# Kernel optimization log

Hardware: AMD Instinct MI355X
Metric: run time of the kernel (lower is better)

The kernel has to match this reference:

```python
import jax, jax.numpy as jnp
import numpy as np

NUM_CLASSES = 10
P_CUTOFF = 0.95
TEMP = 0.5  # temperature used throughout the original forward
B_LB, B_ULB, D = 4096, 6144, 128


def _l2_normalize(x, eps=1e-12):
    # matches torch.nn.functional.normalize(x, dim=1)
    n = jnp.linalg.norm(x, axis=1, keepdims=True)
    return x / jnp.maximum(n, eps)


def setup_inputs() -> dict:
    key = jax.random.key(0)
    k = jax.random.split(key, 6)
    anchor_feat = jax.random.normal(k[0], (B_ULB, D), jnp.float32)
    positive_feat = jax.random.normal(k[1], (B_ULB, D), jnp.float32)
    lb_feat = jax.random.normal(k[2], (B_LB, D), jnp.float32)
    labels = jax.random.randint(k[3], (B_LB,), 0, NUM_CLASSES)
    lb_one_hot = jax.nn.one_hot(labels, NUM_CLASSES, dtype=jnp.float32)
    # scale logits so a realistic fraction of unlabeled samples pass the 0.95 cutoff
    logits_x_ulb_1 = 3.0 * jax.random.normal(k[4], (B_ULB, NUM_CLASSES), jnp.float32)
    logits_x_ulb_2 = 3.0 * jax.random.normal(k[5], (B_ULB, NUM_CLASSES), jnp.float32)
    return {
        "anchor_feat": anchor_feat,
        "positive_feat": positive_feat,
        "lb_feat": lb_feat,
        "lb_one_hot": lb_one_hot,
        "logits_x_ulb_1": logits_x_ulb_1,
        "logits_x_ulb_2": logits_x_ulb_2,
    }


def reference(anchor_feat, positive_feat, lb_feat, lb_one_hot,
              logits_x_ulb_1, logits_x_ulb_2):
    # pick the more-confident view per unlabeled sample
    prob1 = jax.nn.softmax(logits_x_ulb_1 / TEMP, axis=1)
    prob2 = jax.nn.softmax(logits_x_ulb_2 / TEMP, axis=1)
    take1 = jnp.max(prob1, axis=-1) >= jnp.max(prob2, axis=-1)
    logits_gt = jnp.where(take1[:, None], logits_x_ulb_1, logits_x_ulb_2)

    # confidence mask at p_cutoff = 0.95
    mask = (jax.nn.softmax(logits_gt, axis=1) >= P_CUTOFF).astype(logits_gt.dtype)
    logits_gt = logits_gt * mask

    # per-class counts: labeled via one-hot sum; unlabeled via vectorized bincount
    class_num_lb = lb_one_hot.sum(axis=0)
    max_val = jnp.max(logits_gt, axis=1)
    max_idx = jnp.argmax(logits_gt, axis=1)
    valid = (max_val != 0).astype(jnp.float32)  # max_val==0 -> idx -1 -> skipped
    class_num_ulb = jnp.zeros((NUM_CLASSES,), jnp.float32).at[max_idx].add(valid) * 2.0
    class_num = class_num_ulb + class_num_lb

    # build [B_lb + 2*B_ulb, 10] target distribution
    logits_x_ulb = jnp.concatenate([logits_gt, logits_gt], axis=0)
    prob_xulb = jax.nn.softmax(logits_x_ulb / TEMP, axis=-1)
    logits_bf = jnp.concatenate([lb_one_hot, prob_xulb], axis=0)  # [N, 10]

    # self-attention over normalized features (second normalize in the original
    # is idempotent on already unit-norm rows)
    feats = _l2_normalize(jnp.concatenate([lb_feat, anchor_feat, positive_feat], axis=0))  # [N, D]
    attn = jax.nn.softmax(feats @ feats.T / TEMP, axis=1)  # [N, N]
    self_atten = attn @ logits_bf  # [N, 10]

    # per-class division; zero-count classes divided by total count
    denom = jnp.where(class_num == 0, class_num.sum(), class_num)
    logits_af = self_atten / denom[None, :]
    return logits_af
```

## Files before the change

kernel.cpp:

```cpp
#include <hip/hip_runtime.h>
#include <hip/hip_bf16.h>

#define NLB 4096
#define NULB 6144
#define NROWS 16384
#define DD 128
#define NC 10
#define VW 12
#define SEG 16
#define JSEG (NROWS / SEG)
#define BI 256
#define BJ 128
#define SQRTC 1.6986437f
#define FE_BIAS  1.06498747e9f

typedef __bf16 bf16_t;
typedef bf16_t bf16x8 __attribute__((ext_vector_type(8)));
typedef float f32x4 __attribute__((ext_vector_type(4)));
typedef short i16x2 __attribute__((ext_vector_type(2)));
typedef int i32x8 __attribute__((ext_vector_type(8)));
typedef unsigned int u32;
typedef unsigned char u8;

__device__ __forceinline__ size_t f8idx(int row, int c) {
  return ((size_t)(row >> 7) << 14) + (size_t)((row & 127) << 7)
       + (size_t)(((c ^ (row & 7)) & 7) << 4);
}

__device__ __forceinline__ u32 packexp2bf(float c0, float c1) {
#if __has_builtin(__builtin_amdgcn_cvt_pknorm_i16)
  float y0 = fmaf(c0, 1.5259021e-5f, 0.49593857f);
  float y1 = fmaf(c1, 1.5259021e-5f, 0.49593857f);
  union { i16x2 p; u32 u; } cv;
  cv.p = __builtin_amdgcn_cvt_pknorm_i16(y0, y1);
  return cv.u;
#else
  u32 b0 = (u32)(int)fmaf(c0, 32768.0f, FE_BIAS);
  u32 b1 = (u32)(int)fmaf(c1, 32768.0f, FE_BIAS);
  return __builtin_amdgcn_perm(b1, b0, 0x07060302u);
#endif
}

__global__ void kprep2(const float* __restrict__ lb, const float* __restrict__ an,
                       const float* __restrict__ po, const float* __restrict__ onehot,
                       const float* __restrict__ l1, const float* __restrict__ l2,
                       u8* __restrict__ F8, bf16_t* __restrict__ VF,
                       float* __restrict__ clsPart, float* __restrict__ P12) {
  __shared__ float Vtmp[256 * 16];
  __shared__ float lcnt[NC];
  int b = blockIdx.x;
  int t = threadIdx.x;

  if (b < 1024) {
    if (t < 192) P12[(size_t)b * 192 + t] = 0.0f;
    int row = b * 16 + (t >> 4);
    int c = t & 15;
    const float* src;
    if (row < NLB) src = lb + (size_t)row * DD;
    else if (row < NLB + NULB) src = an + (size_t)(row - NLB) * DD;
    else src = po + (size_t)(row - NLB - NULB) * DD;
    float4 v0 = ((const float4*)src)[c * 2];
    float4 v1 = ((const float4*)src)[c * 2 + 1];
    float ss = v0.x*v0.x + v0.y*v0.y + v0.z*v0.z + v0.w*v0.w
             + v1.x*v1.x + v1.y*v1.y + v1.z*v1.z + v1.w*v1.w;
#pragma unroll
    for (int off = 8; off >= 1; off >>= 1) ss += __shfl_xor(ss, off);
    float inv = (16.0f * SQRTC) / fmaxf(sqrtf(ss), 1e-12f);
    u32 d0 = (u32)__builtin_amdgcn_cvt_pk_fp8_f32(v0.x*inv, v0.y*inv, 0, false);
    d0 = (u32)__builtin_amdgcn_cvt_pk_fp8_f32(v0.z*inv, v0.w*inv, d0, true);
    u32 d1 = (u32)__builtin_amdgcn_cvt_pk_fp8_f32(v1.x*inv, v1.y*inv, 0, false);
    d1 = (u32)__builtin_amdgcn_cvt_pk_fp8_f32(v1.z*inv, v1.w*inv, d1, true);
    uint2 dd = {d0, d1};
    *(uint2*)(F8 + f8idx(row, c >> 1) + ((c & 1) << 3)) = dd;
    return;
  }

  if (t < NC) lcnt[t] = 0.0f;
  __syncthreads();
  int gid = (b - 1024) * 256 + t;
  float p[16];
  p[10] = 1.0f; p[11] = 0.f; p[12] = 0.f; p[13] = 0.f; p[14] = 0.f; p[15] = 0.f;
  if (gid < NLB) {
    int idx = 0;
#pragma unroll
    for (int c = 0; c < NC; ++c) {
      p[c] = onehot[(size_t)gid * NC + c];
      if (p[c] == 1.0f) idx = c;
    }
    atomicAdd(&lcnt[idx], 1.0f);
  } else {
    int r = (gid < NLB + NULB) ? (gid - NLB) : (gid - NLB - NULB);
    bool count = (gid < NLB + NULB);
    float a[NC], bb[NC];
#pragma unroll
    for (int c = 0; c < NC; ++c) { a[c] = l1[(size_t)r * NC + c]; bb[c] = l2[(size_t)r * NC + c]; }
    float m1 = a[0], m2 = bb[0];
#pragma unroll
    for (int c = 1; c < NC; ++c) { m1 = fmaxf(m1, a[c]); m2 = fmaxf(m2, bb[c]); }
    float s1 = 0.0f, s2 = 0.0f;
#pragma unroll
    for (int c = 0; c < NC; ++c) {
      s1 += expf(2.0f * (a[c] - m1));
      s2 += expf(2.0f * (bb[c] - m2));
    }
    bool take1 = (s1 <= s2);
    float g[NC];
#pragma unroll
    for (int c = 0; c < NC; ++c) g[c] = take1 ? a[c] : bb[c];
    float mg = g[0];
#pragma unroll
    for (int c = 1; c < NC; ++c) mg = fmaxf(mg, g[c]);
    float e[NC]; float sg = 0.0f;
#pragma unroll
    for (int c = 0; c < NC; ++c) { e[c] = expf(g[c] - mg); sg += e[c]; }
    float msk[NC];
#pragma unroll
    for (int c = 0; c < NC; ++c) msk[c] = ((e[c] / sg) >= 0.95f) ? g[c] : 0.0f;
    float mx = msk[0]; int mi = 0;
#pragma unroll
    for (int c = 1; c < NC; ++c) if (msk[c] > mx) { mx = msk[c]; mi = c; }
    if (count && mx != 0.0f) atomicAdd(&lcnt[mi], 2.0f);
    float mm = 2.0f * msk[0];
#pragma unroll
    for (int c = 1; c < NC; ++c) mm = fmaxf(mm, 2.0f * msk[c]);
    float q[NC]; float sp = 0.0f;
#pragma unroll
    for (int c = 0; c < NC; ++c) { q[c] = expf(2.0f * msk[c] - mm); sp += q[c]; }
#pragma unroll
    for (int c = 0; c < NC; ++c) p[c] = q[c] / sp;
  }
#pragma unroll
  for (int c = 0; c < 16; ++c) Vtmp[t * 16 + c] = p[c];
  __syncthreads();
  if (t < 16) clsPart[(size_t)(b - 1024) * 16 + t] = (t < NC) ? lcnt[t] : 0.0f;
  int gbase = (b - 1024) * 16;
#pragma unroll
  for (int u = 0; u < 4; ++u) {
    int cid = t * 4 + u;
    int gl = cid >> 6;
    int l  = cid & 63;
    int q  = l >> 4;
    int n  = l & 15;
    union { bf16_t h[8]; uint4 uu; } pk;
#pragma unroll
    for (int d = 0; d < 4; ++d) {
      float v = Vtmp[(gl * 16 + q * 4 + d) * 16 + n];
      bf16_t hi = (bf16_t)v;
      pk.h[d] = hi;
      pk.h[4 + d] = (bf16_t)(v - (float)hi);
    }
    *(uint4*)(VF + ((size_t)(gbase + gl) * 64 + l) * 8) = pk.uu;
  }
}

__launch_bounds__(256, 4)
__global__ void kattn(const u8* __restrict__ F8, const bf16_t* __restrict__ VF,
                      float* __restrict__ P12) {
  __shared__ u8 Fs[BJ * 128];
  __shared__ bf16_t Vs[(BJ / 16) * 512];
  int t = threadIdx.x;
  int lane = t & 63;
  int wave = t >> 6;
  int q = lane >> 4;
  int r = lane & 15;
  int i0 = blockIdx.x * BI + wave * 64;
  int jbase = blockIdx.y * JSEG;

  i32x8 bfr[4];
#pragma unroll
  for (int s = 0; s < 4; ++s) {
    int row = i0 + s * 16 + r;
    union { uint4 h[2]; i32x8 v; } bb;
    bb.h[0] = *(const uint4*)(F8 + f8idx(row, 2 * q));
    bb.h[1] = *(const uint4*)(F8 + f8idx(row, 2 * q + 1));
    bfr[s] = bb.v;
  }

  f32x4 acc[4];
#pragma unroll
  for (int s = 0; s < 4; ++s) acc[s] = (f32x4){0.f, 0.f, 0.f, 0.f};
  const f32x4 kZero = {0.f, 0.f, 0.f, 0.f};

  for (int jt = 0; jt < JSEG; jt += BJ) {
    int j0 = jbase + jt;
    __syncthreads();
    {
      const uint4* srcF = (const uint4*)(F8 + ((size_t)(j0 >> 7) << 14));
#pragma unroll
      for (int k = 0; k < 4; ++k) {
        int off = ((k * 4 + wave) << 6) + lane;
        __builtin_amdgcn_global_load_lds(
            (const __attribute__((address_space(1))) uint4*)(srcF + off),
            (__attribute__((address_space(3))) uint4*)((uint4*)Fs + off), 16, 0, 0);
      }
      const uint4* srcV = (const uint4*)(VF + ((size_t)(j0 >> 4) << 9));
#pragma unroll
      for (int k = 0; k < 2; ++k) {
        int off = ((k * 4 + wave) << 6) + lane;
        __builtin_amdgcn_global_load_lds(
            (const __attribute__((address_space(1))) uint4*)(srcV + off),
            (__attribute__((address_space(3))) uint4*)((uint4*)Vs + off), 16, 0, 0);
      }
    }
    __syncthreads();

#pragma unroll
    for (int jj = 0; jj < BJ / 16; ++jj) {
      union { uint4 h[2]; i32x8 v; } af;
      const u8* fsrow = &Fs[(jj * 16 + r) * 128];
      af.h[0] = *(const uint4*)(fsrow + ((((2 * q) ^ (r & 7)) & 7) << 4));
      af.h[1] = *(const uint4*)(fsrow + ((((2 * q + 1) ^ (r & 7)) & 7) << 4));
      bf16x8 bv = *(const bf16x8*)&Vs[jj * 512 + lane * 8];
#pragma unroll
      for (int s = 0; s < 4; ++s) {
        f32x4 cfr = __builtin_amdgcn_mfma_scale_f32_16x16x128_f8f6f4(
            af.v, bfr[s], kZero, 0, 0, 0, 0x7F7F7F7Fu, 0, 0x7F7F7F7Fu);
        union { u32 u[4]; bf16x8 v; } pf;
        pf.u[0] = packexp2bf(cfr[0], cfr[1]);
        pf.u[1] = packexp2bf(cfr[2], cfr[3]);
        pf.u[2] = pf.u[0];
        pf.u[3] = pf.u[1];
        acc[s] = __builtin_amdgcn_mfma_f32_16x16x32_bf16(pf.v, bv, acc[s], 0, 0, 0);
      }
    }
  }

  if (r < 11) {
#pragma unroll
    for (int s = 0; s < 4; ++s) {
      float* op = P12 + (size_t)(i0 + s * 16 + q * 4) * VW + r;
      atomicAdd(&op[0 * VW], acc[s][0]);
      atomicAdd(&op[1 * VW], acc[s][1]);
      atomicAdd(&op[2 * VW], acc[s][2]);
      atomicAdd(&op[3 * VW], acc[s][3]);
    }
  }
}

__global__ void kfinal(float* __restrict__ out, const float* __restrict__ P12,
                       const float* __restrict__ clsPart) {
  __shared__ float clsS[16];
  int t = threadIdx.x;
  if (t < 64) {
    const float4* cp = (const float4*)clsPart;
    float4 c0 = cp[t * 4], c1 = cp[t * 4 + 1], c2 = cp[t * 4 + 2], c3 = cp[t * 4 + 3];
#pragma unroll
    for (int off = 32; off >= 1; off >>= 1) {
      c0.x += __shfl_xor(c0.x, off); c0.y += __shfl_xor(c0.y, off);
      c0.z += __shfl_xor(c0.z, off); c0.w += __shfl_xor(c0.w, off);
      c1.x += __shfl_xor(c1.x, off); c1.y += __shfl_xor(c1.y, off);
      c1.z += __shfl_xor(c1.z, off); c1.w += __shfl_xor(c1.w, off);
      c2.x += __shfl_xor(c2.x, off); c2.y += __shfl_xor(c2.y, off);
    }
    if (t == 0) {
      *(float4*)&clsS[0] = c0;
      *(float4*)&clsS[4] = c1;
      clsS[8] = c2.x; clsS[9] = c2.y;
      clsS[10] = 0.f; clsS[11] = 0.f; clsS[12] = 0.f;
      clsS[13] = 0.f; clsS[14] = 0.f; clsS[15] = 0.f;
    }
  }
  __syncthreads();
  float d[NC]; float tot = 0.0f;
#pragma unroll
  for (int c = 0; c < NC; ++c) { d[c] = clsS[c]; tot += d[c]; }
  int row = blockIdx.x * 256 + t;
  const float* pr = P12 + (size_t)row * VW;
  float rs = 1.0f / pr[10];
  float* op = out + (size_t)row * NC;
#pragma unroll
  for (int c = 0; c < NC; ++c) {
    float den = (d[c] == 0.0f) ? tot : d[c];
    op[c] = pr[c] * rs / den;
  }
}

extern "C" void kernel_launch(void* const* d_in, const int* in_sizes, int n_in,
                              void* d_out, int out_size, void* d_ws, size_t ws_size,
                              hipStream_t stream) {
  const float* anchor   = (const float*)d_in[0];
  const float* positive = (const float*)d_in[1];
  const float* lbfeat   = (const float*)d_in[2];
  const float* onehot   = (const float*)d_in[3];
  const float* l1       = (const float*)d_in[4];
  const float* l2       = (const float*)d_in[5];
  float* out = (float*)d_out;

  char* ws = (char*)d_ws;
  u8*     F8      = (u8*)ws;
  bf16_t* VF      = (bf16_t*)(ws + 2097152);
  float*  P12     = (float*)(ws + 2097152 + 1048576);
  float*  clsPart = (float*)(ws + 2097152 + 1048576 + 786432);

  kprep2<<<1088, 256, 0, stream>>>(lbfeat, anchor, positive, onehot, l1, l2,
                                   F8, VF, clsPart, P12);
  kattn<<<dim3(NROWS / BI, SEG), 256, 0, stream>>>(F8, VF, P12);
  kfinal<<<NROWS / 256, 256, 0, stream>>>(out, P12, clsPart);
}
```

Baseline: 121.4 us.

## Switch P·V to fp16 with two key blocks per MFMA and double-buffer LDS

Replaces the bf16 hi/lo split of the value matrix with a single fp16 value, so each 16x16x32 MFMA now consumes two 16-column key blocks instead of duplicating one. This halves the P·V MFMA count and the V traffic. The fast-exp packing is retuned to emit fp16 bit patterns. The LDS tiles are also double-buffered so the next tile's global-to-LDS load overlaps compute, removing one barrier per iteration. In exchange, fp16 has a narrower exponent range and drops the hi/lo split, which may reduce accuracy, and the loop now hardcodes 8 tiles.

```diff
diff --git a/kernel.cpp b/kernel.cpp
--- a/kernel.cpp
+++ b/kernel.cpp
@@ -15,7 +15,8 @@
 #define FE_BIAS  1.06498747e9f
 
 typedef __bf16 bf16_t;
-typedef bf16_t bf16x8 __attribute__((ext_vector_type(8)));
+typedef _Float16 f16_t;
+typedef f16_t f16x8 __attribute__((ext_vector_type(8)));
 typedef float f32x4 __attribute__((ext_vector_type(4)));
 typedef short i16x2 __attribute__((ext_vector_type(2)));
 typedef int i32x8 __attribute__((ext_vector_type(8)));
@@ -27,24 +28,24 @@
        + (size_t)(((c ^ (row & 7)) & 7) << 4);
 }
 
-__device__ __forceinline__ u32 packexp2bf(float c0, float c1) {
+__device__ __forceinline__ u32 packexp2f16(float c0, float c1) {
 #if __has_builtin(__builtin_amdgcn_cvt_pknorm_i16)
-  float y0 = fmaf(c0, 1.5259021e-5f, 0.49593857f);
-  float y1 = fmaf(c1, 1.5259021e-5f, 0.49593857f);
+  float y0 = fmaf(c0, 1.2207465e-4f, 0.46740490f);
+  float y1 = fmaf(c1, 1.2207465e-4f, 0.46740490f);
   union { i16x2 p; u32 u; } cv;
   cv.p = __builtin_amdgcn_cvt_pknorm_i16(y0, y1);
   return cv.u;
 #else
-  u32 b0 = (u32)(int)fmaf(c0, 32768.0f, FE_BIAS);
-  u32 b1 = (u32)(int)fmaf(c1, 32768.0f, FE_BIAS);
-  return __builtin_amdgcn_perm(b1, b0, 0x07060302u);
+  u32 b0 = (u32)(int)fmaf(c0, 4.0f, 15315.354f);
+  u32 b1 = (u32)(int)fmaf(c1, 4.0f, 15315.354f);
+  return __builtin_amdgcn_perm(b1, b0, 0x05040100u);
 #endif
 }
 
 __global__ void kprep2(const float* __restrict__ lb, const float* __restrict__ an,
                        const float* __restrict__ po, const float* __restrict__ onehot,
                        const float* __restrict__ l1, const float* __restrict__ l2,
-                       u8* __restrict__ F8, bf16_t* __restrict__ VF,
+                       u8* __restrict__ F8, f16_t* __restrict__ VF,
                        float* __restrict__ clsPart, float* __restrict__ P12) {
   __shared__ float Vtmp[256 * 16];
   __shared__ float lcnt[NC];
@@ -133,31 +134,29 @@
   for (int c = 0; c < 16; ++c) Vtmp[t * 16 + c] = p[c];
   __syncthreads();
   if (t < 16) clsPart[(size_t)(b - 1024) * 16 + t] = (t < NC) ? lcnt[t] : 0.0f;
-  int gbase = (b - 1024) * 16;
-#pragma unroll
-  for (int u = 0; u < 4; ++u) {
-    int cid = t * 4 + u;
-    int gl = cid >> 6;
-    int l  = cid & 63;
-    int q  = l >> 4;
-    int n  = l & 15;
-    union { bf16_t h[8]; uint4 uu; } pk;
+  int gbase = (b - 1024) * 8;
+#pragma unroll
+  for (int u = 0; u < 2; ++u) {
+    int cid = u * 256 + t;
+    int G = cid >> 6;
+    int l = cid & 63;
+    int q = l >> 4;
+    int n = l & 15;
+    union { f16_t h[8]; uint4 uu; } pk;
 #pragma unroll
     for (int d = 0; d < 4; ++d) {
-      float v = Vtmp[(gl * 16 + q * 4 + d) * 16 + n];
-      bf16_t hi = (bf16_t)v;
-      pk.h[d] = hi;
-      pk.h[4 + d] = (bf16_t)(v - (float)hi);
-    }
-    *(uint4*)(VF + ((size_t)(gbase + gl) * 64 + l) * 8) = pk.uu;
+      pk.h[d]     = (f16_t)Vtmp[(G * 32      + q * 4 + d) * 16 + n];
+      pk.h[4 + d] = (f16_t)Vtmp[(G * 32 + 16 + q * 4 + d) * 16 + n];
+    }
+    *(uint4*)(VF + ((size_t)(gbase + G) * 64 + l) * 8) = pk.uu;
   }
 }
 
 __launch_bounds__(256, 4)
-__global__ void kattn(const u8* __restrict__ F8, const bf16_t* __restrict__ VF,
+__global__ void kattn(const u8* __restrict__ F8, const f16_t* __restrict__ VF,
                       float* __restrict__ P12) {
-  __shared__ u8 Fs[BJ * 128];
-  __shared__ bf16_t Vs[(BJ / 16) * 512];
+  __shared__ u8 Fs[2][BJ * 128];
+  __shared__ uint4 Vs4[2][256];
   int t = threadIdx.x;
   int lane = t & 63;
   int wave = t >> 6;
@@ -181,49 +180,62 @@
   for (int s = 0; s < 4; ++s) acc[s] = (f32x4){0.f, 0.f, 0.f, 0.f};
   const f32x4 kZero = {0.f, 0.f, 0.f, 0.f};
 
-  for (int jt = 0; jt < JSEG; jt += BJ) {
-    int j0 = jbase + jt;
+  auto stage = [&](int buf, int j0) {
+    const uint4* srcF = (const uint4*)(F8 + ((size_t)(j0 >> 7) << 14));
+#pragma unroll
+    for (int k = 0; k < 4; ++k) {
+      int off = ((k * 4 + wave) << 6) + lane;
+      __builtin_amdgcn_global_load_lds(
+          (const __attribute__((address_space(1))) uint4*)(srcF + off),
+          (__attribute__((address_space(3))) uint4*)((uint4*)Fs[buf] + off), 16, 0, 0);
+    }
+    const uint4* srcV = (const uint4*)VF + ((size_t)(j0 >> 5) << 6);
+    __builtin_amdgcn_global_load_lds(
+        (const __attribute__((address_space(1))) uint4*)(srcV + t),
+        (__attribute__((address_space(3))) uint4*)(Vs4[buf] + t), 16, 0, 0);
+  };
+
+  auto compute = [&](int buf) {
+    const u8* fsb = Fs[buf];
+    const uint4* vsb = Vs4[buf];
+#pragma unroll
+    for (int jp = 0; jp < 4; ++jp) {
+      union { uint4 h[2]; i32x8 v; } afe, afo;
+      const u8* re = fsb + (jp * 32 + r) * 128;
+      const u8* ro = re + 16 * 128;
+      int c0 = (((2 * q) ^ (r & 7)) & 7) << 4;
+      int c1 = (((2 * q + 1) ^ (r & 7)) & 7) << 4;
+      afe.h[0] = *(const uint4*)(re + c0);
+      afe.h[1] = *(const uint4*)(re + c1);
+      afo.h[0] = *(const uint4*)(ro + c0);
+      afo.h[1] = *(const uint4*)(ro + c1);
+      union { uint4 qd; f16x8 v; } bv;
+      bv.qd = vsb[jp * 64 + lane];
+#pragma unroll
+      for (int s = 0; s < 4; ++s) {
+        f32x4 ce = __builtin_amdgcn_mfma_scale_f32_16x16x128_f8f6f4(
+            afe.v, bfr[s], kZero, 0, 0, 0, 0x7F7F7F7Fu, 0, 0x7F7F7F7Fu);
+        f32x4 co = __builtin_amdgcn_mfma_scale_f32_16x16x128_f8f6f4(
+            afo.v, bfr[s], kZero, 0, 0, 0, 0x7F7F7F7Fu, 0, 0x7F7F7F7Fu);
+        union { u32 u[4]; f16x8 v; } pf;
+        pf.u[0] = packexp2f16(ce[0], ce[1]);
+        pf.u[1] = packexp2f16(ce[2], ce[3]);
+        pf.u[2] = packexp2f16(co[0], co[1]);
+        pf.u[3] = packexp2f16(co[2], co[3]);
+        acc[s] = __builtin_amdgcn_mfma_f32_16x16x32_f16(pf.v, bv.v, acc[s], 0, 0, 0);
+      }
+    }
+  };
+
+  stage(0, jbase);
+  __syncthreads();
+#pragma unroll
+  for (int jt = 0; jt < 7; ++jt) {
+    stage((jt + 1) & 1, jbase + (jt + 1) * BJ);
+    compute(jt & 1);
     __syncthreads();
-    {
-      const uint4* srcF = (const uint4*)(F8 + ((size_t)(j0 >> 7) << 14));
-#pragma unroll
-      for (int k = 0; k < 4; ++k) {
-        int off = ((k * 4 + wave) << 6) + lane;
-        __builtin_amdgcn_global_load_lds(
-            (const __attribute__((address_space(1))) uint4*)(srcF + off),
-            (__attribute__((address_space(3))) uint4*)((uint4*)Fs + off), 16, 0, 0);
-      }
-      const uint4* srcV = (const uint4*)(VF + ((size_t)(j0 >> 4) << 9));
-#pragma unroll
-      for (int k = 0; k < 2; ++k) {
-        int off = ((k * 4 + wave) << 6) + lane;
-        __builtin_amdgcn_global_load_lds(
-            (const __attribute__((address_space(1))) uint4*)(srcV + off),
-            (__attribute__((address_space(3))) uint4*)((uint4*)Vs + off), 16, 0, 0);
-      }
-    }
-    __syncthreads();
-
-#pragma unroll
-    for (int jj = 0; jj < BJ / 16; ++jj) {
-      union { uint4 h[2]; i32x8 v; } af;
-      const u8* fsrow = &Fs[(jj * 16 + r) * 128];
-      af.h[0] = *(const uint4*)(fsrow + ((((2 * q) ^ (r & 7)) & 7) << 4));
-      af.h[1] = *(const uint4*)(fsrow + ((((2 * q + 1) ^ (r & 7)) & 7) << 4));
-      bf16x8 bv = *(const bf16x8*)&Vs[jj * 512 + lane * 8];
-#pragma unroll
-      for (int s = 0; s < 4; ++s) {
-        f32x4 cfr = __builtin_amdgcn_mfma_scale_f32_16x16x128_f8f6f4(
-            af.v, bfr[s], kZero, 0, 0, 0, 0x7F7F7F7Fu, 0, 0x7F7F7F7Fu);
-        union { u32 u[4]; bf16x8 v; } pf;
-        pf.u[0] = packexp2bf(cfr[0], cfr[1]);
-        pf.u[1] = packexp2bf(cfr[2], cfr[3]);
-        pf.u[2] = pf.u[0];
-        pf.u[3] = pf.u[1];
-        acc[s] = __builtin_amdgcn_mfma_f32_16x16x32_bf16(pf.v, bv, acc[s], 0, 0, 0);
-      }
-    }
-  }
+  }
+  compute(1);
 
   if (r < 11) {
 #pragma unroll
@@ -288,9 +300,9 @@
 
   char* ws = (char*)d_ws;
   u8*     F8      = (u8*)ws;
-  bf16_t* VF      = (bf16_t*)(ws + 2097152);
-  float*  P12     = (float*)(ws + 2097152 + 1048576);
-  float*  clsPart = (float*)(ws + 2097152 + 1048576 + 786432);
+  f16_t*  VF      = (f16_t*)(ws + 2097152);
+  float*  P12     = (float*)(ws + 2097152 + 524288);
+  float*  clsPart = (float*)(ws + 2097152 + 524288 + 786432);
 
   kprep2<<<1088, 256, 0, stream>>>(lbfeat, anchor, positive, onehot, l1, l2,
                                    F8, VF, clsPart, P12);
```

After: 113.4 us. 1.07x faster.
